# Performance work log

Measured on AMD Instinct MI355X. Metric: run time of the kernel, lower is better.

## Reference

```python
import jax, jax.numpy as jnp
import numpy as np

B, T_IN, T_OUT, N, D_IN, D_OUT, H, L, K = 32, 12, 12, 200, 2, 1, 128, 2, 2
DH = H // 2
M = 2 * K + 1  # identity + K diffusion steps for each of the 2 supports
SQRT_H = float(np.sqrt(H))


def setup_inputs():
    key = jax.random.key(0)
    ks = iter(jax.random.split(key, 40))
    def rn(shape, s=0.1):
        return jax.random.normal(next(ks), shape, dtype=jnp.float32) * s
    return {
        "encoder_inputs": rn((B, T_IN, N, D_IN), 1.0),
        "decoder_inputs": rn((B, T_OUT, N, D_OUT), 1.0),
        "gru_Wih": rn((3 * H, D_IN)), "gru_Whh": rn((3 * H, H)),
        "gru_bih": rn((3 * H,)), "gru_bhh": rn((3 * H,)),
        "att_W": rn((DH, H)), "att_b": rn((DH,)),
        "w_len_C": rn((DH, 1)), "w_key": rn((H, DH)), "w_query": rn((H, DH)),
        "enc_Wg0": rn(((D_IN + H) * M, 2 * H)), "enc_bg0": rn((2 * H,)),
        "enc_Wc0": rn(((D_IN + H) * M, H)), "enc_bc0": rn((H,)),
        "enc_Wg1": rn((2 * H * M, 2 * H)), "enc_bg1": rn((2 * H,)),
        "enc_Wc1": rn((2 * H * M, H)), "enc_bc1": rn((H,)),
        "dec_Wg0": rn(((D_OUT + H) * M, 2 * H)), "dec_bg0": rn((2 * H,)),
        "dec_Wc0": rn(((D_OUT + H) * M, H)), "dec_bc0": rn((H,)),
        "dec_Wg1": rn((2 * H * M, 2 * H)), "dec_bg1": rn((2 * H,)),
        "dec_Wc1": rn((2 * H * M, H)), "dec_bc1": rn((H,)),
        "proj_W": rn((D_OUT, H)), "proj_b": rn((D_OUT,)),
        "top_k": 20,
    }


def _gconv(supports, x, W, b):
    # x: (B, N, D); supports: list of (B, N, N). Chebyshev-style diffusion.
    xs = [x]
    for s in supports:
        x0, x1 = x, jnp.einsum('bij,bjd->bid', s, x)
        xs.append(x1)
        for _ in range(2, K + 1):
            x2 = 2.0 * jnp.einsum('bij,bjd->bid', s, x1) - x0
            xs.append(x2)
            x0, x1 = x1, x2
    xm = jnp.stack(xs, axis=-1).reshape(x.shape[0], x.shape[1], -1)  # (B,N,D*M)
    return xm @ W + b


def _cell(supports, inp, h, Wg, bg, Wc, bc):
    # DCGRU cell: diffusion-conv GRU gating. inp (B,N,di), h (B,N,H)
    ru = jax.nn.sigmoid(_gconv(supports, jnp.concatenate([inp, h], -1), Wg, bg))
    r, u = ru[..., :H], ru[..., H:]
    c = jnp.tanh(_gconv(supports, jnp.concatenate([inp, r * h], -1), Wc, bc))
    return u * h + (1.0 - u) * c


def _supports(x, gru_Wih, gru_Whh, gru_bih, gru_bhh, att_W, att_b, w_len_C, w_key, w_query, top_k):
    # x: (B, T, N, D) -> per-node GRU over time (fold nodes into batch)
    xt = jnp.transpose(x, (1, 2, 0, 3)).reshape(T_IN, N * B, D_IN)
    def gru_step(h, xin):
        gi = xin @ gru_Wih.T + gru_bih
        gh = h @ gru_Whh.T + gru_bhh
        ir, iz, ig = jnp.split(gi, 3, -1)
        hr, hz, hg = jnp.split(gh, 3, -1)
        r = jax.nn.sigmoid(ir + hr)
        z = jax.nn.sigmoid(iz + hz)
        n = jnp.tanh(ig + r * hg)
        hnew = (1.0 - z) * n + z * h
        return hnew, hnew
    _, outs = jax.lax.scan(gru_step, jnp.zeros((N * B, H), x.dtype), xt)
    outs = outs.reshape(T_IN, N, B, H)
    # temporal attention pooling per node
    sc = jax.nn.relu(jnp.einsum('tnbh,dh->tnbd', outs, att_W) + att_b)
    att_t = jax.nn.softmax(jnp.einsum('tnbd,do->tnbo', sc, w_len_C)[..., 0], axis=0)  # (T,N,B)
    pooled = jnp.einsum('tnbh,tnb->bnh', outs, att_t)  # (B,N,H)
    # node-node attention -> sparsified adjacency
    keym = pooled @ w_key
    qm = pooled @ w_query
    attn = jax.nn.softmax(jnp.einsum('bnd,bmd->bnm', keym, qm) / SQRT_H, axis=-1)
    kth = jax.lax.top_k(attn, top_k)[0][..., -1:]  # k-th largest per row
    adj = jnp.where(attn >= kth, attn, 0.0) + jnp.eye(N, dtype=attn.dtype)
    def rw(a):  # D^-1 A, row-normalized random walk
        d = a.sum(-1)
        dinv = jnp.where(d == 0.0, 0.0, 1.0 / d)
        return dinv[..., None] * a
    s1 = jnp.transpose(rw(adj), (0, 2, 1))
    s2 = jnp.transpose(rw(jnp.transpose(adj, (0, 2, 1))), (0, 2, 1))
    return [s1, s2]


def _forward(encoder_inputs, decoder_inputs, gru_Wih, gru_Whh, gru_bih, gru_bhh,
             att_W, att_b, w_len_C, w_key, w_query,
             enc_Wg0, enc_bg0, enc_Wc0, enc_bc0, enc_Wg1, enc_bg1, enc_Wc1, enc_bc1,
             dec_Wg0, dec_bg0, dec_Wc0, dec_bc0, dec_Wg1, dec_bg1, dec_Wc1, dec_bc1,
             proj_W, proj_b, top_k):
    supports = _supports(encoder_inputs, gru_Wih, gru_Whh, gru_bih, gru_bhh,
                         att_W, att_b, w_len_C, w_key, w_query, top_k)
    enc = jnp.transpose(encoder_inputs, (1, 0, 2, 3))  # (T,B,N,Din)
    enc_params = [(enc_Wg0, enc_bg0, enc_Wc0, enc_bc0), (enc_Wg1, enc_bg1, enc_Wc1, enc_bc1)]
    dec_params = [(dec_Wg0, dec_bg0, dec_Wc0, dec_bc0), (dec_Wg1, dec_bg1, dec_Wc1, dec_bc1)]
    # encoder: scan over time per layer
    cur = enc
    hiddens = []
    for l in range(L):
        Wg, bg, Wc, bc = enc_params[l]
        def estep(h, xin, Wg=Wg, bg=bg, Wc=Wc, bc=bc):
            hn = _cell(supports, xin, h, Wg, bg, Wc, bc)
            return hn, hn
        hl, cur = jax.lax.scan(estep, jnp.zeros((B, N, H), enc.dtype), cur)
        hiddens.append(hl)
    go = jnp.zeros((B, N, D_OUT), enc.dtype)
    def dstep(carry, _):
        hs, x = carry
        hs_new = []
        for l in range(L):
            hn = _cell(supports, x, hs[l], *dec_params[l])
            x = hn
            hs_new.append(hn)
        proj = x @ proj_W.T + proj_b  # (B,N,D_OUT)
        return (tuple(hs_new), proj), proj.reshape(B, N * D_OUT)
    _, outputs = jax.lax.scan(dstep, (tuple(hiddens), go), None, length=T_OUT)
    return outputs  # (T_OUT, B, N*D_OUT)


def reference(encoder_inputs, decoder_inputs, gru_Wih, gru_Whh, gru_bih, gru_bhh,
              att_W, att_b, w_len_C, w_key, w_query,
              enc_Wg0, enc_bg0, enc_Wc0, enc_bc0, enc_Wg1, enc_bg1, enc_Wc1, enc_bc1,
              dec_Wg0, dec_bg0, dec_Wc0, dec_bc0, dec_Wg1, dec_bg1, dec_Wc1, dec_bc1,
              proj_W, proj_b, top_k):
    return _forward(encoder_inputs, decoder_inputs, gru_Wih, gru_Whh, gru_bih, gru_bhh,
                    att_W, att_b, w_len_C, w_key, w_query,
                    enc_Wg0, enc_bg0, enc_Wc0, enc_bc0, enc_Wg1, enc_bg1, enc_Wc1, enc_bc1,
                    dec_Wg0, dec_bg0, dec_Wc0, dec_bc0, dec_Wg1, dec_bg1, dec_Wc1, dec_bc1,
                    proj_W, proj_b, top_k)
```

## Files before the change

### kernel.cpp

```cpp
#include <hip/hip_runtime.h>
#include <hip/hip_bf16.h>
#include <math.h>

#define BB 32
#define T_INC 12
#define T_OUTC 12
#define NN 200
#define DIN0 2
#define HH 128
#define DHALF 64
#define NB (NN*BB)
#define XROW 256
#define MSTRIDE ((size_t)NB*XROW)
#define CHUNK 32
#define QT 2
#define KT2 7
#define RT2 13
#define SFRAG_PER_B ((size_t)RT2*KT2*64*8)
#define PANEL_E (KT2*QT*64*8)
#define GCONV_LDS6 (6*PANEL_E*2)
#define GRU_ROWS 16
#define INV_SQRT_H 0.08838834764831845f

typedef __attribute__((ext_vector_type(8))) short bf16x8;
typedef __attribute__((ext_vector_type(4))) float f32x4;

__device__ __forceinline__ float sigmf(float x){ return 1.f/(1.f+expf(-x)); }
__device__ __forceinline__ float bfu(uint32_t b){ union{uint32_t u;float f;}v; v.u=b<<16; return v.f; }
__device__ __forceinline__ uint32_t fbf(float f){ union{float f2;uint32_t u;}v; v.f2=f; return (v.u + 0x7fffu + ((v.u>>16)&1u))>>16; }
__device__ __forceinline__ void splitbf(float v, uint32_t& hi, uint32_t& lo){
  hi = fbf(v);
  lo = fbf(v - bfu(hi));
}

__global__ void k_whhT(const float* __restrict__ Whh, float* __restrict__ WT) {
  int idx = blockIdx.x*256 + threadIdx.x;
  if (idx >= 3*HH*HH) return;
  int i3 = idx / HH; int k = idx % HH;
  WT[(size_t)k*(3*HH) + i3] = Whh[idx];
}

__global__ void k_wshuf(const float* __restrict__ W, __hip_bfloat16* __restrict__ Wfh,
                        __hip_bfloat16* __restrict__ Wfl, int d, int d_pad, int OUT) {
  int idx = blockIdx.x*256 + threadIdx.x;
  int total = 5*d_pad*OUT;
  if (idx >= total) return;
  int o = idx % OUT; int tmp = idx / OUT; int k = tmp % d_pad; int m = tmp / d_pad;
  float v = (k < d) ? W[((size_t)k*5 + m)*OUT + o] : 0.f;
  int kt = k >> 5, kr = k & 31;
  int lane = ((kr>>3)<<4) | (o & 15);
  int j = kr & 7;
  int nt = o >> 4;
  int KT = d_pad >> 5, NT = OUT >> 4;
  size_t addr = ((((size_t)m*KT + kt)*NT + nt)*64 + (size_t)lane)*8 + j;
  uint32_t hi, lo; splitbf(v, hi, lo);
  Wfh[addr] = *(__hip_bfloat16*)&hi;
  Wfl[addr] = *(__hip_bfloat16*)&lo;
}

__global__ void k_sshuf(const float* __restrict__ adj, const float* __restrict__ rs,
                        const float* __restrict__ cs,
                        __hip_bfloat16* __restrict__ SFH, __hip_bfloat16* __restrict__ SFL) {
  const int PER_B = 208*224;
  int idx = blockIdx.x*256 + threadIdx.x;
  if (idx >= 2*BB*PER_B) return;
  int e = idx % PER_B; int t2 = idx / PER_B; int b = t2 % BB; int mat = t2 / BB;
  int n = e / 224; int j = e % 224;
  float v = 0.f;
  if (n < NN && j < NN) {
    if (mat == 0) v = adj[((size_t)b*NN + j)*NN + n] / rs[(size_t)b*NN + j];
    else          v = adj[((size_t)b*NN + n)*NN + j] / cs[(size_t)b*NN + j];
  }
  int rt = n >> 4, rr = n & 15, kt = j >> 5, kr = j & 31;
  int lane = ((kr >> 3) << 4) | rr;
  int jj = kr & 7;
  size_t addr = ((size_t)(mat*BB + b)*RT2*KT2 + (size_t)(rt*KT2 + kt))*512
              + (size_t)lane*8 + jj;
  uint32_t hi, lo; splitbf(v, hi, lo);
  SFH[addr] = *(__hip_bfloat16*)&hi;
  SFL[addr] = *(__hip_bfloat16*)&lo;
}

__global__ __launch_bounds__(512) void k_gru_all(
    const float* __restrict__ enc_in, const float* __restrict__ Wih,
    const float* __restrict__ WhhT, const float* __restrict__ bih,
    const float* __restrict__ bhh, float* __restrict__ outs) {
  int row0 = blockIdx.x * GRU_ROWS;
  int tid = threadIdx.x;
  int g = tid >> 7;
  int i = tid & 127;
  __shared__ float hs[GRU_ROWS][HH];
  #pragma unroll
  for (int j=0;j<4;j++) hs[g+4*j][i] = 0.f;
  float wi0 = Wih[(0*HH+i)*2+0], wi1 = Wih[(0*HH+i)*2+1];
  float wz0 = Wih[(1*HH+i)*2+0], wz1 = Wih[(1*HH+i)*2+1];
  float wg0 = Wih[(2*HH+i)*2+0], wg1 = Wih[(2*HH+i)*2+1];
  float bi = bih[i], bz = bih[HH+i], bg = bih[2*HH+i];
  float bhr = bhh[i], bhz = bhh[HH+i], bhg = bhh[2*HH+i];
  int nn_[4], bb_[4];
  #pragma unroll
  for (int j=0;j<4;j++) { int r = row0 + g + 4*j; nn_[j] = r / BB; bb_[j] = r % BB; }
  for (int t=0;t<T_INC;t++) {
    __syncthreads();
    float hr[4], hz[4], hg[4], ii_[4], iz_[4], ig_[4];
    #pragma unroll
    for (int j=0;j<4;j++) {
      float x0 = enc_in[(((size_t)bb_[j]*T_INC + t)*NN + nn_[j])*DIN0 + 0];
      float x1 = enc_in[(((size_t)bb_[j]*T_INC + t)*NN + nn_[j])*DIN0 + 1];
      ii_[j] = wi0*x0 + wi1*x1 + bi;
      iz_[j] = wz0*x0 + wz1*x1 + bz;
      ig_[j] = wg0*x0 + wg1*x1 + bg;
      hr[j] = bhr; hz[j] = bhz; hg[j] = bhg;
    }
    for (int k=0;k<HH;k++) {
      const float* wr = WhhT + (size_t)k*(3*HH);
      float w0 = wr[i], w1 = wr[i+128], w2 = wr[i+256];
      #pragma unroll
      for (int j=0;j<4;j++) {
        float hv = hs[g+4*j][k];
        hr[j] += w0*hv; hz[j] += w1*hv; hg[j] += w2*hv;
      }
    }
    float hn[4];
    #pragma unroll
    for (int j=0;j<4;j++) {
      float r = sigmf(ii_[j]+hr[j]);
      float z = sigmf(iz_[j]+hz[j]);
      float nn2 = tanhf(ig_[j] + r*hg[j]);
      hn[j] = (1.f-z)*nn2 + z*hs[g+4*j][i];
    }
    __syncthreads();
    #pragma unroll
    for (int j=0;j<4;j++) {
      hs[g+4*j][i] = hn[j];
      outs[(((size_t)t*NN+nn_[j])*BB+bb_[j])*HH + i] = hn[j];
    }
  }
}

__global__ __launch_bounds__(256) void k_att_pool(
    const float* __restrict__ outs, const float* __restrict__ attW,
    const float* __restrict__ attb, const float* __restrict__ wlc,
    float* __restrict__ pooled) {
  int row = blockIdx.x; int n = row / BB, b = row % BB;
  int tid = threadIdx.x;
  __shared__ float o_s[T_INC][HH];
  __shared__ float aw[DHALF][HH+1];
  __shared__ float pt[T_INC];
  for (int i = tid; i < T_INC*HH; i += 256) {
    int t = i >> 7, k = i & 127;
    o_s[t][k] = outs[(((size_t)t*NN+n)*BB+b)*HH + k];
  }
  for (int i = tid; i < DHALF*HH; i += 256) {
    int d2 = i >> 7, k = i & 127;
    aw[d2][k] = attW[(size_t)d2*HH + k];
  }
  __syncthreads();
  int d = tid & 63, tq = tid >> 6;
  float ab = attb[d], wc = wlc[d];
  float part[3];
  #pragma unroll
  for (int j=0;j<3;j++) {
    int t = tq + j*4;
    float acc = ab;
    for (int k=0;k<HH;k++) acc += aw[d][k]*o_s[t][k];
    part[j] = fmaxf(acc, 0.f)*wc;
  }
  for (int off=32; off; off>>=1)
    #pragma unroll
    for (int j=0;j<3;j++) part[j] += __shfl_xor(part[j], off, 64);
  if (d == 0) { pt[tq] = part[0]; pt[tq+4] = part[1]; pt[tq+8] = part[2]; }
  __syncthreads();
  float mx = -1e30f;
  for (int t=0;t<T_INC;t++) mx = fmaxf(mx, pt[t]);
  float e[T_INC]; float s = 0.f;
  for (int t=0;t<T_INC;t++) { e[t] = expf(pt[t]-mx); s += e[t]; }
  float inv = 1.f/s;
  for (int k=tid;k<HH;k+=256) {
    float acc = 0.f;
    for (int t=0;t<T_INC;t++) acc += o_s[t][k]*e[t];
    pooled[((size_t)b*NN+n)*HH + k] = acc*inv;
  }
}

__global__ void k_keyquery(const float* __restrict__ pooled, const float* __restrict__ wkey,
                           const float* __restrict__ wqry, float* __restrict__ keym,
                           float* __restrict__ qm) {
  int bn = blockIdx.x; int lane = threadIdx.x;
  __shared__ float p_s[HH];
  p_s[lane] = pooled[(size_t)bn*HH + lane];
  p_s[lane+64] = pooled[(size_t)bn*HH + lane + 64];
  __syncthreads();
  float ka = 0.f, qa = 0.f;
  for (int k=0;k<HH;k++) {
    float pv = p_s[k];
    ka += pv*wkey[(size_t)k*DHALF + lane];
    qa += pv*wqry[(size_t)k*DHALF + lane];
  }
  keym[(size_t)bn*DHALF + lane] = ka;
  qm[(size_t)bn*DHALF + lane] = qa;
}

__global__ void k_attn_row(const float* __restrict__ keym, const float* __restrict__ qm,
                           const int* __restrict__ topkp, float* __restrict__ adj,
                           float* __restrict__ rowsum) {
  int bn = blockIdx.x; int b = bn / NN; int n = bn % NN;
  int tid = threadIdx.x;
  __shared__ float key_s[DHALF];
  __shared__ float attv[256];
  __shared__ float red[256];
  __shared__ int redi[256];
  if (tid < DHALF) key_s[tid] = keym[(size_t)bn*DHALF + tid];
  __syncthreads();
  float sc = -1e30f;
  if (tid < NN) {
    float a = 0.f;
    const float* qrow = qm + ((size_t)b*NN + tid)*DHALF;
    for (int k=0;k<DHALF;k++) a += key_s[k]*qrow[k];
    sc = a * INV_SQRT_H;
  }
  red[tid] = sc; __syncthreads();
  for (int s=128;s>0;s>>=1){ if (tid<s) red[tid]=fmaxf(red[tid],red[tid+s]); __syncthreads(); }
  float mx = red[0]; __syncthreads();
  float e = (tid<NN) ? expf(sc-mx) : 0.f;
  red[tid] = e; __syncthreads();
  for (int s=128;s>0;s>>=1){ if (tid<s) red[tid]+=red[tid+s]; __syncthreads(); }
  float inv = 1.f/red[0]; __syncthreads();
  float av = e*inv;
  attv[tid] = (tid<NN) ? av : -1e30f;
  __syncthreads();
  int Ks = topkp[0]; if (Ks > NN) Ks = NN;
  float kth = -1e30f;
  for (int it=0; it<Ks; it++) {
    red[tid] = attv[tid]; redi[tid] = tid; __syncthreads();
    for (int s=128;s>0;s>>=1){
      if (tid<s && red[tid+s] > red[tid]) { red[tid]=red[tid+s]; redi[tid]=redi[tid+s]; }
      __syncthreads();
    }
    kth = red[0];
    if (tid==0) attv[redi[0]] = -1e30f;
    __syncthreads();
  }
  float aout = 0.f;
  if (tid < NN) {
    aout = (av >= kth) ? av : 0.f;
    if (tid == n) aout += 1.f;
    adj[((size_t)b*NN+n)*NN + tid] = aout;
  }
  red[tid] = aout; __syncthreads();
  for (int s=128;s>0;s>>=1){ if (tid<s) red[tid]+=red[tid+s]; __syncthreads(); }
  if (tid==0) rowsum[bn] = red[0];
}

__global__ void k_colsum(const float* __restrict__ adj, float* __restrict__ cs) {
  int b = blockIdx.x;
  for (int j=threadIdx.x; j<NN; j+=blockDim.x) {
    float s = 0.f;
    for (int i=0;i<NN;i++) s += adj[((size_t)b*NN+i)*NN + j];
    cs[(size_t)b*NN + j] = s;
  }
}

__global__ __launch_bounds__(512) void k_gconv_mfma(
    const float* __restrict__ x, int bs, int ns, int din,
    const float* __restrict__ h, const float* __restrict__ ru,
    const __hip_bfloat16* __restrict__ SFH, const __hip_bfloat16* __restrict__ SFL,
    uint32_t* __restrict__ XP, int d) {
  extern __shared__ char ldsc[];
  ushort* X0H = (ushort*)ldsc;
  ushort* X0L = X0H + PANEL_E;
  ushort* T1H = X0L + PANEL_E;
  ushort* T1L = T1H + PANEL_E;
  ushort* T2H = T1L + PANEL_E;
  ushort* T2L = T2H + PANEL_E;
  int c0 = blockIdx.x*CHUNK;
  int b  = blockIdx.y;
  int tid = threadIdx.x;
  int l = tid & 63, wid = tid >> 6;

  { uint4 z = make_uint4(0,0,0,0);
    uint4* p = (uint4*)ldsc;
    for (int i = tid; i < GCONV_LDS6/16; i += 512) p[i] = z; }
  __syncthreads();

  for (int i = tid; i < NN*CHUNK; i += 512) {
    int n = i >> 5, cc = i & 31;
    int c = c0 + cc;
    float v = 0.f;
    if (c < din) {
      v = x[(size_t)b*bs + (size_t)n*ns + c];
    } else if (c < d) {
      int k = c - din;
      v = h[((size_t)(b*NN+n))*HH + k];
      if (ru) v *= ru[(size_t)(b*NN+n)*256 + k];
    }
    uint32_t hi, lo; splitbf(v, hi, lo);
    int kt = n >> 5, kr = n & 31;
    int ln = ((kr>>3)<<4) | (cc & 15), jj = kr & 7, q = cc >> 4;
    int fa = ((kt*QT + q)*64 + ln)*8 + jj;
    X0H[fa] = (ushort)hi; X0L[fa] = (ushort)lo;
    XP[(size_t)(b*NN+n)*XROW + c] = hi | (lo << 16);
  }
  __syncthreads();

  for (int task = wid; task < 2*RT2; task += 8) {
    int side = task & 1, rt = task >> 1;
    const __hip_bfloat16* AH = SFH + (size_t)(side*BB + b)*SFRAG_PER_B;
    const __hip_bfloat16* AL = SFL + (size_t)(side*BB + b)*SFRAG_PER_B;
    ushort* TH = side ? T2H : T1H;
    ushort* TL = side ? T2L : T1L;
    int mout = 1 + 2*side;
    f32x4 acc[QT];
    #pragma unroll
    for (int q=0;q<QT;q++) acc[q] = (f32x4){0.f,0.f,0.f,0.f};
    for (int kt = 0; kt < KT2; kt++) {
      size_t aoff = ((size_t)(rt*KT2+kt)*64 + l)*8;
      bf16x8 ah = *(const bf16x8*)(AH + aoff);
      bf16x8 al = *(const bf16x8*)(AL + aoff);
      #pragma unroll
      for (int q=0;q<QT;q++) {
        int boff = ((kt*QT+q)*64 + l)*8;
        bf16x8 bh = *(const bf16x8*)(X0H + boff);
        bf16x8 bl = *(const bf16x8*)(X0L + boff);
        acc[q] = __builtin_amdgcn_mfma_f32_16x16x32_bf16(ah, bl, acc[q], 0, 0, 0);
        acc[q] = __builtin_amdgcn_mfma_f32_16x16x32_bf16(al, bh, acc[q], 0, 0, 0);
        acc[q] = __builtin_amdgcn_mfma_f32_16x16x32_bf16(ah, bh, acc[q], 0, 0, 0);
      }
    }
    int colb = l & 15;
    #pragma unroll
    for (int q=0;q<QT;q++) {
      int cc = q*16 + colb;
      #pragma unroll
      for (int r=0;r<4;r++) {
        int n = rt*16 + ((l>>4)<<2) + r;
        float v = acc[q][r];
        int kt2 = n >> 5, kr = n & 31;
        int ln = ((kr>>3)<<4) | colb, jj = kr & 7;
        int fa = ((kt2*QT + q)*64 + ln)*8 + jj;
        uint32_t hi, lo; splitbf(v, hi, lo);
        TH[fa] = (ushort)hi; TL[fa] = (ushort)lo;
        if (n < NN)
          XP[(size_t)mout*MSTRIDE + (size_t)(b*NN+n)*XROW + c0 + cc] = hi | (lo << 16);
      }
    }
  }
  __syncthreads();

  for (int task = wid; task < 2*RT2; task += 8) {
    int side = task & 1, rt = task >> 1;
    const __hip_bfloat16* AH = SFH + (size_t)(side*BB + b)*SFRAG_PER_B;
    const __hip_bfloat16* AL = SFL + (size_t)(side*BB + b)*SFRAG_PER_B;
    const ushort* BH = side ? T2H : T1H;
    const ushort* BL = side ? T2L : T1L;
    int mout = 2 + 2*side;
    f32x4 acc[QT];
    #pragma unroll
    for (int q=0;q<QT;q++) acc[q] = (f32x4){0.f,0.f,0.f,0.f};
    for (int kt = 0; kt < KT2; kt++) {
      size_t aoff = ((size_t)(rt*KT2+kt)*64 + l)*8;
      bf16x8 ah = *(const bf16x8*)(AH + aoff);
      bf16x8 al = *(const bf16x8*)(AL + aoff);
      #pragma unroll
      for (int q=0;q<QT;q++) {
        int boff = ((kt*QT+q)*64 + l)*8;
        bf16x8 bh = *(const bf16x8*)(BH + boff);
        bf16x8 bl = *(const bf16x8*)(BL + boff);
        acc[q] = __builtin_amdgcn_mfma_f32_16x16x32_bf16(ah, bl, acc[q], 0, 0, 0);
        acc[q] = __builtin_amdgcn_mfma_f32_16x16x32_bf16(al, bh, acc[q], 0, 0, 0);
        acc[q] = __builtin_amdgcn_mfma_f32_16x16x32_bf16(ah, bh, acc[q], 0, 0, 0);
      }
    }
    int colb = l & 15;
    #pragma unroll
    for (int q=0;q<QT;q++) {
      int cc = q*16 + colb;
      #pragma unroll
      for (int r=0;r<4;r++) {
        int n = rt*16 + ((l>>4)<<2) + r;
        float v = acc[q][r];
        int kt2 = n >> 5, kr = n & 31;
        int ln = ((kr>>3)<<4) | colb, jj = kr & 7;
        int fa = ((kt2*QT + q)*64 + ln)*8 + jj;
        uint32_t h2 = X0H[fa], l2 = X0L[fa];
        v = 2.f*v - (bfu(h2) + bfu(l2));
        uint32_t hi, lo; splitbf(v, hi, lo);
        if (n < NN)
          XP[(size_t)mout*MSTRIDE + (size_t)(b*NN+n)*XROW + c0 + cc] = hi | (lo << 16);
      }
    }
  }
}

template<int OUT, int PATH>
__global__ __launch_bounds__(256) void k_dense_mfma(
    const uint32_t* __restrict__ XP,
    const __hip_bfloat16* __restrict__ Wfh, const __hip_bfloat16* __restrict__ Wfl,
    const float* __restrict__ bias, int d_pad,
    float* __restrict__ RU, const float* __restrict__ h, float* __restrict__ hnew,
    const float* __restrict__ pW, const float* __restrict__ pb,
    float* __restrict__ out, float* __restrict__ decx, int t) {
  constexpr int ROWS  = (PATH==0) ? 32 : 16;
  constexpr int NQ    = (PATH==0) ? 4  : 2;
  constexpr int MAXIT = (PATH==0) ? 4  : 2;
  __shared__ ushort SA[2][2*ROWS*256];
  int tid = threadIdx.x;
  int w = tid >> 6, l = tid & 63;
  int rblk = blockIdx.x*ROWS;
  int rbase = (PATH==0) ? (w&1)*16 : 0;
  int cbase = (PATH==0) ? ((int)blockIdx.y*128 + (w>>1)*64) : (w*NQ*16);
  const int NT = OUT >> 4;
  int KT = d_pad >> 5;
  f32x4 acc[NQ];
  #pragma unroll
  for (int q=0;q<NQ;q++) acc[q] = (f32x4){0.f,0.f,0.f,0.f};
  size_t boff = (((size_t)(cbase>>4))*64 + l)*8;
  int ngrp = d_pad >> 3;
  int total = ROWS*ngrp;
  uint4 pf0[MAXIT], pf1[MAXIT];

  auto issue = [&](int m){
    int c2 = 0;
    for (int i2 = tid; i2 < total; i2 += 256, c2++) {
      int r = i2 / ngrp, cg = i2 % ngrp;
      const uint32_t* gp = XP + (size_t)m*MSTRIDE + (size_t)(rblk+r)*XROW + cg*8;
      pf0[c2] = *(const uint4*)gp;
      pf1[c2] = *(const uint4*)(gp+4);
    }
  };
  auto commit = [&](int buf){
    ushort* SAh = SA[buf];
    ushort* SAl = SA[buf] + ROWS*256;
    int c2 = 0;
    for (int i2 = tid; i2 < total; i2 += 256, c2++) {
      int r = i2 / ngrp, cg = i2 % ngrp;
      uint4 p0 = pf0[c2], p1 = pf1[c2];
      uint4 hv, lv;
      hv.x = (p0.x & 0xffffu) | (p0.y << 16);
      hv.y = (p0.z & 0xffffu) | (p0.w << 16);
      hv.z = (p1.x & 0xffffu) | (p1.y << 16);
      hv.w = (p1.z & 0xffffu) | (p1.w << 16);
      lv.x = (p0.x >> 16) | (p0.y & 0xffff0000u);
      lv.y = (p0.z >> 16) | (p0.w & 0xffff0000u);
      lv.z = (p1.x >> 16) | (p1.y & 0xffff0000u);
      lv.w = (p1.z >> 16) | (p1.w & 0xffff0000u);
      uint32_t bo2 = ((uint32_t)(r*256 + cg*8)*2) ^ ((uint32_t)(r&7)<<4);
      *(uint4*)((char*)SAh + bo2) = hv;
      *(uint4*)((char*)SAl + bo2) = lv;
    }
  };

  issue(0); commit(0);
  for (int m=0;m<5;m++) {
    if (m < 4) issue(m+1);
    __syncthreads();
    const ushort* SAh = SA[m&1];
    const ushort* SAl = SA[m&1] + ROWS*256;
    for (int kt=0; kt<KT; kt++) {
      int rr = rbase + (l & 15);
      uint32_t fb = ((uint32_t)(rr*256 + kt*32 + (l>>4)*8)*2) ^ ((uint32_t)(rr&7)<<4);
      bf16x8 ah = *(const bf16x8*)((const char*)SAh + fb);
      bf16x8 al = *(const bf16x8*)((const char*)SAl + fb);
      size_t bo = boff + ((size_t)(m*KT + kt)*NT)*512;
      #pragma unroll
      for (int q=0;q<NQ;q++) {
        bf16x8 bh = *(const bf16x8*)(Wfh + bo + (size_t)q*512);
        bf16x8 bl = *(const bf16x8*)(Wfl + bo + (size_t)q*512);
        acc[q] = __builtin_amdgcn_mfma_f32_16x16x32_bf16(ah, bl, acc[q], 0, 0, 0);
        acc[q] = __builtin_amdgcn_mfma_f32_16x16x32_bf16(al, bh, acc[q], 0, 0, 0);
        acc[q] = __builtin_amdgcn_mfma_f32_16x16x32_bf16(ah, bh, acc[q], 0, 0, 0);
      }
    }
    if (m < 4) commit((m+1)&1);
  }
  bool doproj = (PATH==1) && (pW != nullptr);
  if (doproj) __syncthreads();
  float* PH = (float*)SA;
  int drow0 = rbase + ((l>>4)<<2);
  int col0 = l & 15;
  #pragma unroll
  for (int q=0;q<NQ;q++) {
    int col = cbase + q*16 + col0;
    float bv = bias[col];
    #pragma unroll
    for (int r=0;r<4;r++) {
      int rowrel = drow0 + r;
      int row = rblk + rowrel;
      float v = acc[q][r] + bv;
      if (PATH==0) {
        RU[(size_t)row*256 + col] = sigmf(v);
      } else {
        float c = tanhf(v);
        float u = RU[(size_t)row*256 + 128 + col];
        float hv = u*h[(size_t)row*HH + col] + (1.f-u)*c;
        hnew[(size_t)row*HH + col] = hv;
        if (doproj) PH[rowrel*HH + col] = hv;
      }
    }
  }
  if (doproj) {
    __syncthreads();
    int rowrel = tid >> 4;
    int sub = tid & 15;
    float s = 0.f;
    const float* ph = PH + rowrel*HH + sub*8;
    #pragma unroll
    for (int c=0;c<8;c++) s += ph[c]*pW[sub*8 + c];
    s += __shfl_xor(s, 1, 64);
    s += __shfl_xor(s, 2, 64);
    s += __shfl_xor(s, 4, 64);
    s += __shfl_xor(s, 8, 64);
    if (sub == 0) {
      float pv = s + pb[0];
      int gr = rblk + rowrel;
      out[(size_t)t*NB + gr] = pv;
      decx[gr] = pv;
    }
  }
}

extern "C" void kernel_launch(void* const* d_in, const int* in_sizes, int n_in,
                              void* d_out, int out_size, void* d_ws, size_t ws_size,
                              hipStream_t stream) {
  const float* enc_in = (const float*)d_in[0];
  const float* gWih = (const float*)d_in[2];
  const float* gWhh = (const float*)d_in[3];
  const float* gbih = (const float*)d_in[4];
  const float* gbhh = (const float*)d_in[5];
  const float* attW = (const float*)d_in[6];
  const float* attb = (const float*)d_in[7];
  const float* wlc  = (const float*)d_in[8];
  const float* wkey = (const float*)d_in[9];
  const float* wqry = (const float*)d_in[10];
  const float* cWg[4] = {(const float*)d_in[11],(const float*)d_in[15],(const float*)d_in[19],(const float*)d_in[23]};
  const float* cbg[4] = {(const float*)d_in[12],(const float*)d_in[16],(const float*)d_in[20],(const float*)d_in[24]};
  const float* cWc[4] = {(const float*)d_in[13],(const float*)d_in[17],(const float*)d_in[21],(const float*)d_in[25]};
  const float* cbc[4] = {(const float*)d_in[14],(const float*)d_in[18],(const float*)d_in[22],(const float*)d_in[26]};
  const float* pW = (const float*)d_in[27];
  const float* pb = (const float*)d_in[28];
  const int* topkp = (const int*)d_in[29];
  float* out = (float*)d_out;

  const int d_full[4] = {130, 256, 129, 256};
  const int d_padv[4] = {192, 256, 192, 256};

  float* ws = (float*)d_ws;
  size_t off = 0;
  auto alloc = [&](size_t n) { float* p = ws + off; off += (n + 255) & ~(size_t)255; return p; };

  float* RS   = alloc(NB);
  float* CS   = alloc(NB);
  float* RU   = alloc((size_t)NB*256);
  float* H0A  = alloc((size_t)NB*HH);
  float* H0B  = alloc((size_t)NB*HH);
  float* H1A  = alloc((size_t)NB*HH);
  float* H1B  = alloc((size_t)NB*HH);
  float* DECX = alloc(NB);
  float* WHHT = alloc((size_t)3*HH*HH);
  __hip_bfloat16* SFH = (__hip_bfloat16*)alloc((size_t)2*BB*SFRAG_PER_B/2);
  __hip_bfloat16* SFL = (__hip_bfloat16*)alloc((size_t)2*BB*SFRAG_PER_B/2);
  __hip_bfloat16 *WGFh[4], *WGFl[4], *WCFh[4], *WCFl[4];
  for (int p=0;p<4;p++) {
    WGFh[p] = (__hip_bfloat16*)alloc((size_t)5*d_padv[p]*256/2);
    WGFl[p] = (__hip_bfloat16*)alloc((size_t)5*d_padv[p]*256/2);
    WCFh[p] = (__hip_bfloat16*)alloc((size_t)5*d_padv[p]*128/2);
    WCFl[p] = (__hip_bfloat16*)alloc((size_t)5*d_padv[p]*128/2);
  }

  const size_t SUP_SZ = (size_t)T_INC*NN*BB*HH
                      + (size_t)NB*HH
                      + (size_t)NB*DHALF*2
                      + (size_t)BB*NN*NN + 4096;
  const size_t CELL_SZ = 5*MSTRIDE + 4096;
  float* UNION = alloc(SUP_SZ > CELL_SZ ? SUP_SZ : CELL_SZ);
  float* OUTS = UNION;
  float* POOL = OUTS + (size_t)T_INC*NN*BB*HH;
  float* KEYM = POOL + (size_t)NB*HH;
  float* QMM  = KEYM + (size_t)NB*DHALF;
  float* ADJ  = QMM  + (size_t)NB*DHALF;
  uint32_t* XP = (uint32_t*)UNION;

  if (off*sizeof(float) > ws_size) return;

  hipMemsetAsync(H0A, 0, (size_t)NB*HH*sizeof(float), stream);
  hipMemsetAsync(H1A, 0, (size_t)NB*HH*sizeof(float), stream);
  hipMemsetAsync(DECX, 0, (size_t)NB*sizeof(float), stream);

  k_whhT<<<(3*HH*HH+255)/256, 256, 0, stream>>>(gWhh, WHHT);
  for (int p=0;p<4;p++) {
    int tg = 5*d_padv[p]*256;
    k_wshuf<<<(tg+255)/256, 256, 0, stream>>>(cWg[p], WGFh[p], WGFl[p], d_full[p], d_padv[p], 256);
    int tc = 5*d_padv[p]*128;
    k_wshuf<<<(tc+255)/256, 256, 0, stream>>>(cWc[p], WCFh[p], WCFl[p], d_full[p], d_padv[p], 128);
  }

  k_gru_all<<<NB/GRU_ROWS, 512, 0, stream>>>(enc_in, gWih, WHHT, gbih, gbhh, OUTS);
  k_att_pool<<<NB, 256, 0, stream>>>(OUTS, attW, attb, wlc, POOL);
  k_keyquery<<<NB, 64, 0, stream>>>(POOL, wkey, wqry, KEYM, QMM);
  k_attn_row<<<NB, 256, 0, stream>>>(KEYM, QMM, topkp, ADJ, RS);
  k_colsum<<<BB, 256, 0, stream>>>(ADJ, CS);
  { int tot = 2*BB*208*224;
    k_sshuf<<<(tot+255)/256, 256, 0, stream>>>(ADJ, RS, CS, SFH, SFL); }

  auto gconv = [&](const float* x, int bs, int ns, int din, const float* hcur,
                   const float* ru, int pidx) {
    int d = d_full[pidx], dp = d_padv[pidx];
    dim3 gg(dp/CHUNK, BB);
    k_gconv_mfma<<<gg, 512, GCONV_LDS6, stream>>>(
        x, bs, ns, din, hcur, ru, SFH, SFL, XP, d);
  };

  auto cell = [&](const float* x, int bs, int ns, int din,
                  float** hcur, float** halt, int pidx, int t) {
    int dp = d_padv[pidx];
    gconv(x, bs, ns, din, *hcur, nullptr, pidx);
    k_dense_mfma<256,0><<<dim3(NB/32,2),256,0,stream>>>(
        XP, WGFh[pidx], WGFl[pidx], cbg[pidx], dp, RU, nullptr, nullptr,
        nullptr, nullptr, nullptr, nullptr, 0);
    gconv(x, bs, ns, din, *hcur, RU, pidx);
    const float* ppW = (pidx == 3) ? pW : nullptr;
    k_dense_mfma<128,1><<<dim3(NB/16,1),256,0,stream>>>(
        XP, WCFh[pidx], WCFl[pidx], cbc[pidx], dp, RU, *hcur, *halt,
        ppW, pb, out, DECX, t);
    float* tswp = *hcur; *hcur = *halt; *halt = tswp;
  };

  float* h0cur = H0A; float* h0alt = H0B;
  float* h1cur = H1A; float* h1alt = H1B;

  for (int t=0;t<T_INC;t++) {
    cell(enc_in + (size_t)t*NN*DIN0, T_INC*NN*DIN0, DIN0, DIN0, &h0cur, &h0alt, 0, 0);
    cell(h0cur, NN*HH, HH, HH, &h1cur, &h1alt, 1, 0);
  }
  for (int t=0;t<T_OUTC;t++) {
    cell(DECX, NN, 1, 1, &h0cur, &h0alt, 2, t);
    cell(h0cur, NN*HH, HH, HH, &h1cur, &h1alt, 3, t);
  }
}
```

Measured before the change: 9.123 ms.

## Fuse recurrent DCGRU cell loop into a persistent megakernel with grid barriers

Replaces the 192 per-timestep launches (two gconv and two dense launches per cell) with a single persistent kernel of 256 blocks. The blocks walk all encoder and decoder cells and separate phases with a software grid barrier built on atomics. The dense gate and candidate phases are re-tiled to 32-row tasks over 512 threads so that one block covers all output columns. This is meant to remove kernel launch gaps and tail idle time. In exchange it relies on all 256 blocks being co-resident, adds a barrier cost at every phase, and runs fewer, larger blocks than the separate kernels did.

```diff
diff --git a/kernel.cpp b/kernel.cpp
--- a/kernel.cpp
+++ b/kernel.cpp
@@ -18,7 +18,8 @@
 #define RT2 13
 #define SFRAG_PER_B ((size_t)RT2*KT2*64*8)
 #define PANEL_E (KT2*QT*64*8)
-#define GCONV_LDS6 (6*PANEL_E*2)
+#define MEGA_LDS (6*PANEL_E*2)
+#define NBLK 256
 #define GRU_ROWS 16
 #define INV_SQRT_H 0.08838834764831845f
 
@@ -31,6 +32,24 @@
 __device__ __forceinline__ void splitbf(float v, uint32_t& hi, uint32_t& lo){
   hi = fbf(v);
   lo = fbf(v - bfu(hi));
+}
+
+__device__ __forceinline__ void gridbar(int* cnt, int* gen) {
+  __syncthreads();
+  if (threadIdx.x == 0) {
+    __threadfence();
+    int g = __hip_atomic_load(gen, __ATOMIC_ACQUIRE, __HIP_MEMORY_SCOPE_AGENT);
+    int old = __hip_atomic_fetch_add(cnt, 1, __ATOMIC_ACQ_REL, __HIP_MEMORY_SCOPE_AGENT);
+    if (old == NBLK-1) {
+      __hip_atomic_store(cnt, 0, __ATOMIC_RELAXED, __HIP_MEMORY_SCOPE_AGENT);
+      __hip_atomic_fetch_add(gen, 1, __ATOMIC_ACQ_REL, __HIP_MEMORY_SCOPE_AGENT);
+    } else {
+      while (__hip_atomic_load(gen, __ATOMIC_ACQUIRE, __HIP_MEMORY_SCOPE_AGENT) == g)
+        __builtin_amdgcn_s_sleep(2);
+    }
+    __threadfence();
+  }
+  __syncthreads();
 }
 
 __global__ void k_whhT(const float* __restrict__ Whh, float* __restrict__ WT) {
@@ -261,26 +280,28 @@
   }
 }
 
-__global__ __launch_bounds__(512) void k_gconv_mfma(
+
+__device__ void ph_gconv(char* ldsc, int task,
     const float* __restrict__ x, int bs, int ns, int din,
     const float* __restrict__ h, const float* __restrict__ ru,
     const __hip_bfloat16* __restrict__ SFH, const __hip_bfloat16* __restrict__ SFL,
-    uint32_t* __restrict__ XP, int d) {
-  extern __shared__ char ldsc[];
+    uint32_t* __restrict__ XP, int d, int dp) {
+  int nch = dp / CHUNK;
+  if (task >= nch*BB) return;
+  int c0 = (task % nch)*CHUNK;
+  int b  = task / nch;
   ushort* X0H = (ushort*)ldsc;
   ushort* X0L = X0H + PANEL_E;
   ushort* T1H = X0L + PANEL_E;
   ushort* T1L = T1H + PANEL_E;
   ushort* T2H = T1L + PANEL_E;
   ushort* T2L = T2H + PANEL_E;
-  int c0 = blockIdx.x*CHUNK;
-  int b  = blockIdx.y;
   int tid = threadIdx.x;
   int l = tid & 63, wid = tid >> 6;
 
   { uint4 z = make_uint4(0,0,0,0);
     uint4* p = (uint4*)ldsc;
-    for (int i = tid; i < GCONV_LDS6/16; i += 512) p[i] = z; }
+    for (int i = tid; i < (6*PANEL_E*2)/16; i += 512) p[i] = z; }
   __syncthreads();
 
   for (int i = tid; i < NN*CHUNK; i += 512) {
@@ -303,8 +324,8 @@
   }
   __syncthreads();
 
-  for (int task = wid; task < 2*RT2; task += 8) {
-    int side = task & 1, rt = task >> 1;
+  for (int task2 = wid; task2 < 2*RT2; task2 += 8) {
+    int side = task2 & 1, rt = task2 >> 1;
     const __hip_bfloat16* AH = SFH + (size_t)(side*BB + b)*SFRAG_PER_B;
     const __hip_bfloat16* AL = SFL + (size_t)(side*BB + b)*SFRAG_PER_B;
     ushort* TH = side ? T2H : T1H;
@@ -347,8 +368,8 @@
   }
   __syncthreads();
 
-  for (int task = wid; task < 2*RT2; task += 8) {
-    int side = task & 1, rt = task >> 1;
+  for (int task2 = wid; task2 < 2*RT2; task2 += 8) {
+    int side = task2 & 1, rt = task2 >> 1;
     const __hip_bfloat16* AH = SFH + (size_t)(side*BB + b)*SFRAG_PER_B;
     const __hip_bfloat16* AL = SFL + (size_t)(side*BB + b)*SFRAG_PER_B;
     const ushort* BH = side ? T2H : T1H;
@@ -392,36 +413,30 @@
   }
 }
 
-template<int OUT, int PATH>
-__global__ __launch_bounds__(256) void k_dense_mfma(
+__device__ void ph_dense_gate(char* ldsc, int task,
     const uint32_t* __restrict__ XP,
     const __hip_bfloat16* __restrict__ Wfh, const __hip_bfloat16* __restrict__ Wfl,
-    const float* __restrict__ bias, int d_pad,
-    float* __restrict__ RU, const float* __restrict__ h, float* __restrict__ hnew,
-    const float* __restrict__ pW, const float* __restrict__ pb,
-    float* __restrict__ out, float* __restrict__ decx, int t) {
-  constexpr int ROWS  = (PATH==0) ? 32 : 16;
-  constexpr int NQ    = (PATH==0) ? 4  : 2;
-  constexpr int MAXIT = (PATH==0) ? 4  : 2;
-  __shared__ ushort SA[2][2*ROWS*256];
+    const float* __restrict__ bias, int dp, float* __restrict__ RU) {
+  if (task >= NB/32) return;
   int tid = threadIdx.x;
   int w = tid >> 6, l = tid & 63;
-  int rblk = blockIdx.x*ROWS;
-  int rbase = (PATH==0) ? (w&1)*16 : 0;
-  int cbase = (PATH==0) ? ((int)blockIdx.y*128 + (w>>1)*64) : (w*NQ*16);
-  const int NT = OUT >> 4;
-  int KT = d_pad >> 5;
-  f32x4 acc[NQ];
+  int rblk = task*32;
+  int rbase = (w&1)*16;
+  int cbase = (w>>1)*64;
+  const int NT = 16;
+  int KT = dp >> 5;
+  f32x4 acc[4];
   #pragma unroll
-  for (int q=0;q<NQ;q++) acc[q] = (f32x4){0.f,0.f,0.f,0.f};
+  for (int q=0;q<4;q++) acc[q] = (f32x4){0.f,0.f,0.f,0.f};
   size_t boff = (((size_t)(cbase>>4))*64 + l)*8;
-  int ngrp = d_pad >> 3;
-  int total = ROWS*ngrp;
-  uint4 pf0[MAXIT], pf1[MAXIT];
+  int ngrp = dp >> 3;
+  int total = 32*ngrp;
+  uint4 pf0[2], pf1[2];
+  ushort* SA0 = (ushort*)ldsc;
 
   auto issue = [&](int m){
     int c2 = 0;
-    for (int i2 = tid; i2 < total; i2 += 256, c2++) {
+    for (int i2 = tid; i2 < total; i2 += 512, c2++) {
       int r = i2 / ngrp, cg = i2 % ngrp;
       const uint32_t* gp = XP + (size_t)m*MSTRIDE + (size_t)(rblk+r)*XROW + cg*8;
       pf0[c2] = *(const uint4*)gp;
@@ -429,10 +444,10 @@
     }
   };
   auto commit = [&](int buf){
-    ushort* SAh = SA[buf];
-    ushort* SAl = SA[buf] + ROWS*256;
+    ushort* SAh = SA0 + buf*(2*32*256);
+    ushort* SAl = SAh + 32*256;
     int c2 = 0;
-    for (int i2 = tid; i2 < total; i2 += 256, c2++) {
+    for (int i2 = tid; i2 < total; i2 += 512, c2++) {
       int r = i2 / ngrp, cg = i2 % ngrp;
       uint4 p0 = pf0[c2], p1 = pf1[c2];
       uint4 hv, lv;
@@ -454,8 +469,8 @@
   for (int m=0;m<5;m++) {
     if (m < 4) issue(m+1);
     __syncthreads();
-    const ushort* SAh = SA[m&1];
-    const ushort* SAl = SA[m&1] + ROWS*256;
+    const ushort* SAh = SA0 + (m&1)*(2*32*256);
+    const ushort* SAl = SAh + 32*256;
     for (int kt=0; kt<KT; kt++) {
       int rr = rbase + (l & 15);
       uint32_t fb = ((uint32_t)(rr*256 + kt*32 + (l>>4)*8)*2) ^ ((uint32_t)(rr&7)<<4);
@@ -463,7 +478,7 @@
       bf16x8 al = *(const bf16x8*)((const char*)SAl + fb);
       size_t bo = boff + ((size_t)(m*KT + kt)*NT)*512;
       #pragma unroll
-      for (int q=0;q<NQ;q++) {
+      for (int q=0;q<4;q++) {
         bf16x8 bh = *(const bf16x8*)(Wfh + bo + (size_t)q*512);
         bf16x8 bl = *(const bf16x8*)(Wfl + bo + (size_t)q*512);
         acc[q] = __builtin_amdgcn_mfma_f32_16x16x32_bf16(ah, bl, acc[q], 0, 0, 0);
@@ -473,29 +488,116 @@
     }
     if (m < 4) commit((m+1)&1);
   }
-  bool doproj = (PATH==1) && (pW != nullptr);
-  if (doproj) __syncthreads();
-  float* PH = (float*)SA;
   int drow0 = rbase + ((l>>4)<<2);
   int col0 = l & 15;
   #pragma unroll
-  for (int q=0;q<NQ;q++) {
+  for (int q=0;q<4;q++) {
+    int col = cbase + q*16 + col0;
+    float bv = bias[col];
+    #pragma unroll
+    for (int r=0;r<4;r++) {
+      int row = rblk + drow0 + r;
+      RU[(size_t)row*256 + col] = sigmf(acc[q][r] + bv);
+    }
+  }
+}
+
+__device__ void ph_dense_cand(char* ldsc, int task,
+    const uint32_t* __restrict__ XP,
+    const __hip_bfloat16* __restrict__ Wfh, const __hip_bfloat16* __restrict__ Wfl,
+    const float* __restrict__ bias, int dp,
+    const float* __restrict__ RU, const float* __restrict__ h, float* __restrict__ hnew,
+    const float* __restrict__ pW, const float* __restrict__ pb,
+    float* __restrict__ out, float* __restrict__ decx, int t) {
+  if (task >= NB/32) return;
+  int tid = threadIdx.x;
+  int w = tid >> 6, l = tid & 63;
+  int rblk = task*32;
+  int rbase = (w&1)*16;
+  int cbase = (w>>1)*32;
+  const int NT = 8;
+  int KT = dp >> 5;
+  f32x4 acc[2];
+  #pragma unroll
+  for (int q=0;q<2;q++) acc[q] = (f32x4){0.f,0.f,0.f,0.f};
+  size_t boff = (((size_t)(cbase>>4))*64 + l)*8;
+  int ngrp = dp >> 3;
+  int total = 32*ngrp;
+  uint4 pf0[2], pf1[2];
+  ushort* SA0 = (ushort*)ldsc;
+
+  auto issue = [&](int m){
+    int c2 = 0;
+    for (int i2 = tid; i2 < total; i2 += 512, c2++) {
+      int r = i2 / ngrp, cg = i2 % ngrp;
+      const uint32_t* gp = XP + (size_t)m*MSTRIDE + (size_t)(rblk+r)*XROW + cg*8;
+      pf0[c2] = *(const uint4*)gp;
+      pf1[c2] = *(const uint4*)(gp+4);
+    }
+  };
+  auto commit = [&](int buf){
+    ushort* SAh = SA0 + buf*(2*32*256);
+    ushort* SAl = SAh + 32*256;
+    int c2 = 0;
+    for (int i2 = tid; i2 < total; i2 += 512, c2++) {
+      int r = i2 / ngrp, cg = i2 % ngrp;
+      uint4 p0 = pf0[c2], p1 = pf1[c2];
+      uint4 hv, lv;
+      hv.x = (p0.x & 0xffffu) | (p0.y << 16);
+      hv.y = (p0.z & 0xffffu) | (p0.w << 16);
+      hv.z = (p1.x & 0xffffu) | (p1.y << 16);
+      hv.w = (p1.z & 0xffffu) | (p1.w << 16);
+      lv.x = (p0.x >> 16) | (p0.y & 0xffff0000u);
+      lv.y = (p0.z >> 16) | (p0.w & 0xffff0000u);
+      lv.z = (p1.x >> 16) | (p1.y & 0xffff0000u);
+      lv.w = (p1.z >> 16) | (p1.w & 0xffff0000u);
+      uint32_t bo2 = ((uint32_t)(r*256 + cg*8)*2) ^ ((uint32_t)(r&7)<<4);
+      *(uint4*)((char*)SAh + bo2) = hv;
+      *(uint4*)((char*)SAl + bo2) = lv;
+    }
+  };
+
+  issue(0); commit(0);
+  for (int m=0;m<5;m++) {
+    if (m < 4) issue(m+1);
+    __syncthreads();
+    const ushort* SAh = SA0 + (m&1)*(2*32*256);
+    const ushort* SAl = SAh + 32*256;
+    for (int kt=0; kt<KT; kt++) {
+      int rr = rbase + (l & 15);
+      uint32_t fb = ((uint32_t)(rr*256 + kt*32 + (l>>4)*8)*2) ^ ((uint32_t)(rr&7)<<4);
+      bf16x8 ah = *(const bf16x8*)((const char*)SAh + fb);
+      bf16x8 al = *(const bf16x8*)((const char*)SAl + fb);
+      size_t bo = boff + ((size_t)(m*KT + kt)*NT)*512;
+      #pragma unroll
+      for (int q=0;q<2;q++) {
+        bf16x8 bh = *(const bf16x8*)(Wfh + bo + (size_t)q*512);
+        bf16x8 bl = *(const bf16x8*)(Wfl + bo + (size_t)q*512);
+        acc[q] = __builtin_amdgcn_mfma_f32_16x16x32_bf16(ah, bl, acc[q], 0, 0, 0);
+        acc[q] = __builtin_amdgcn_mfma_f32_16x16x32_bf16(al, bh, acc[q], 0, 0, 0);
+        acc[q] = __builtin_amdgcn_mfma_f32_16x16x32_bf16(ah, bh, acc[q], 0, 0, 0);
+      }
+    }
+    if (m < 4) commit((m+1)&1);
+  }
+  bool doproj = (pW != nullptr);
+  if (doproj) __syncthreads();
+  float* PH = (float*)ldsc;
+  int drow0 = rbase + ((l>>4)<<2);
+  int col0 = l & 15;
+  #pragma unroll
+  for (int q=0;q<2;q++) {
     int col = cbase + q*16 + col0;
     float bv = bias[col];
     #pragma unroll
     for (int r=0;r<4;r++) {
       int rowrel = drow0 + r;
       int row = rblk + rowrel;
-      float v = acc[q][r] + bv;
-      if (PATH==0) {
-        RU[(size_t)row*256 + col] = sigmf(v);
-      } else {
-        float c = tanhf(v);
-        float u = RU[(size_t)row*256 + 128 + col];
-        float hv = u*h[(size_t)row*HH + col] + (1.f-u)*c;
-        hnew[(size_t)row*HH + col] = hv;
-        if (doproj) PH[rowrel*HH + col] = hv;
-      }
+      float c = tanhf(acc[q][r] + bv);
+      float u = RU[(size_t)row*256 + 128 + col];
+      float hv = u*h[(size_t)row*HH + col] + (1.f-u)*c;
+      hnew[(size_t)row*HH + col] = hv;
+      if (doproj) PH[rowrel*HH + col] = hv;
     }
   }
   if (doproj) {
@@ -516,6 +618,51 @@
       out[(size_t)t*NB + gr] = pv;
       decx[gr] = pv;
     }
+  }
+}
+
+struct MegaP {
+  const float* enc_in;
+  const __hip_bfloat16 *SFH, *SFL;
+  uint32_t* XP;
+  float *RU, *H0A, *H0B, *H1A, *H1B, *DECX, *out;
+  const float *pW, *pb;
+  const __hip_bfloat16 *WGFh[4], *WGFl[4], *WCFh[4], *WCFl[4];
+  const float *cbg[4], *cbc[4];
+  int* bar;
+};
+
+__global__ __launch_bounds__(512, 1) void k_mega(MegaP P) {
+  extern __shared__ char ldsc[];
+  int task = blockIdx.x;
+  const int d_full[4] = {130, 256, 129, 256};
+  const int d_padv[4] = {192, 256, 192, 256};
+  float* h0cur = P.H0A; float* h0alt = P.H0B;
+  float* h1cur = P.H1A; float* h1alt = P.H1B;
+
+  auto cell = [&](const float* x, int bs, int ns, int din,
+                  float*& hc, float*& ha, int pidx, int t) {
+    int d = d_full[pidx], dp = d_padv[pidx];
+    ph_gconv(ldsc, task, x, bs, ns, din, hc, nullptr, P.SFH, P.SFL, P.XP, d, dp);
+    gridbar(P.bar, P.bar+1);
+    ph_dense_gate(ldsc, task, P.XP, P.WGFh[pidx], P.WGFl[pidx], P.cbg[pidx], dp, P.RU);
+    gridbar(P.bar, P.bar+1);
+    ph_gconv(ldsc, task, x, bs, ns, din, hc, P.RU, P.SFH, P.SFL, P.XP, d, dp);
+    gridbar(P.bar, P.bar+1);
+    const float* ppW = (pidx == 3) ? P.pW : nullptr;
+    ph_dense_cand(ldsc, task, P.XP, P.WCFh[pidx], P.WCFl[pidx], P.cbc[pidx], dp,
+                  P.RU, hc, ha, ppW, P.pb, P.out, P.DECX, t);
+    gridbar(P.bar, P.bar+1);
+    float* tmp = hc; hc = ha; ha = tmp;
+  };
+
+  for (int t=0;t<T_INC;t++) {
+    cell(P.enc_in + (size_t)t*NN*DIN0, T_INC*NN*DIN0, DIN0, DIN0, h0cur, h0alt, 0, 0);
+    cell(h0cur, NN*HH, HH, HH, h1cur, h1alt, 1, 0);
+  }
+  for (int t=0;t<T_OUTC;t++) {
+    cell(P.DECX, NN, 1, 1, h0cur, h0alt, 2, t);
+    cell(h0cur, NN*HH, HH, HH, h1cur, h1alt, 3, t);
   }
 }
 
@@ -557,6 +704,7 @@
   float* H1B  = alloc((size_t)NB*HH);
   float* DECX = alloc(NB);
   float* WHHT = alloc((size_t)3*HH*HH);
+  int*   BAR  = (int*)alloc(256);
   __hip_bfloat16* SFH = (__hip_bfloat16*)alloc((size_t)2*BB*SFRAG_PER_B/2);
   __hip_bfloat16* SFL = (__hip_bfloat16*)alloc((size_t)2*BB*SFRAG_PER_B/2);
   __hip_bfloat16 *WGFh[4], *WGFl[4], *WCFh[4], *WCFl[4];
@@ -585,6 +733,7 @@
   hipMemsetAsync(H0A, 0, (size_t)NB*HH*sizeof(float), stream);
   hipMemsetAsync(H1A, 0, (size_t)NB*HH*sizeof(float), stream);
   hipMemsetAsync(DECX, 0, (size_t)NB*sizeof(float), stream);
+  hipMemsetAsync(BAR, 0, 256*sizeof(float), stream);
 
   k_whhT<<<(3*HH*HH+255)/256, 256, 0, stream>>>(gWhh, WHHT);
   for (int p=0;p<4;p++) {
@@ -602,38 +751,15 @@
   { int tot = 2*BB*208*224;
     k_sshuf<<<(tot+255)/256, 256, 0, stream>>>(ADJ, RS, CS, SFH, SFL); }
 
-  auto gconv = [&](const float* x, int bs, int ns, int din, const float* hcur,
-                   const float* ru, int pidx) {
-    int d = d_full[pidx], dp = d_padv[pidx];
-    dim3 gg(dp/CHUNK, BB);
-    k_gconv_mfma<<<gg, 512, GCONV_LDS6, stream>>>(
-        x, bs, ns, din, hcur, ru, SFH, SFL, XP, d);
-  };
-
-  auto cell = [&](const float* x, int bs, int ns, int din,
-                  float** hcur, float** halt, int pidx, int t) {
-    int dp = d_padv[pidx];
-    gconv(x, bs, ns, din, *hcur, nullptr, pidx);
-    k_dense_mfma<256,0><<<dim3(NB/32,2),256,0,stream>>>(
-        XP, WGFh[pidx], WGFl[pidx], cbg[pidx], dp, RU, nullptr, nullptr,
-        nullptr, nullptr, nullptr, nullptr, 0);
-    gconv(x, bs, ns, din, *hcur, RU, pidx);
-    const float* ppW = (pidx == 3) ? pW : nullptr;
-    k_dense_mfma<128,1><<<dim3(NB/16,1),256,0,stream>>>(
-        XP, WCFh[pidx], WCFl[pidx], cbc[pidx], dp, RU, *hcur, *halt,
-        ppW, pb, out, DECX, t);
-    float* tswp = *hcur; *hcur = *halt; *halt = tswp;
-  };
-
-  float* h0cur = H0A; float* h0alt = H0B;
-  float* h1cur = H1A; float* h1alt = H1B;
-
-  for (int t=0;t<T_INC;t++) {
-    cell(enc_in + (size_t)t*NN*DIN0, T_INC*NN*DIN0, DIN0, DIN0, &h0cur, &h0alt, 0, 0);
-    cell(h0cur, NN*HH, HH, HH, &h1cur, &h1alt, 1, 0);
-  }
-  for (int t=0;t<T_OUTC;t++) {
-    cell(DECX, NN, 1, 1, &h0cur, &h0alt, 2, t);
-    cell(h0cur, NN*HH, HH, HH, &h1cur, &h1alt, 3, t);
-  }
-}
+  MegaP P;
+  P.enc_in = enc_in; P.SFH = SFH; P.SFL = SFL; P.XP = XP;
+  P.RU = RU; P.H0A = H0A; P.H0B = H0B; P.H1A = H1A; P.H1B = H1B;
+  P.DECX = DECX; P.out = out; P.pW = pW; P.pb = pb;
+  for (int p=0;p<4;p++) {
+    P.WGFh[p] = WGFh[p]; P.WGFl[p] = WGFl[p];
+    P.WCFh[p] = WCFh[p]; P.WCFl[p] = WCFl[p];
+    P.cbg[p] = cbg[p]; P.cbc[p] = cbc[p];
+  }
+  P.bar = BAR;
+  k_mega<<<NBLK, 512, MEGA_LDS, stream>>>(P);
+}
```

After: 23.76 ms. 160% more time.
